# Optimization experiments

Hardware: AMD Instinct MI355X
Metric: run time of the kernel (lower is better)

The kernel has to match this reference:

```python
import jax, jax.numpy as jnp
import numpy as np

N = 50000      # num nodes
E = 1_600_000  # num edges
D = 64         # in_dim == hidden_dim
H = 4          # heads
C = 16         # head_dim = hidden_dim // heads
NEG = 0.2      # leaky_relu negative slope (PyG GATConv default)


def setup_inputs() -> dict:
    key = jax.random.key(0)
    ks = jax.random.split(key, 20)
    f = lambda k, s: (jax.random.normal(k, s, jnp.float32) * 0.1)
    return dict(
        node_features=jax.random.normal(ks[0], (N, D), jnp.float32),
        edge_index=jax.random.randint(ks[1], (2, E), 0, N, dtype=jnp.int32),
        edge_type=jax.random.randint(ks[2], (E,), 0, 5, dtype=jnp.int32),
        edge_attr=jax.random.normal(ks[3], (E, 1), jnp.float32),
        # GAT layer 1 (PyG GATConv: lin has no bias, att_* are [H,C], final bias [H*C])
        W1=f(ks[4], (D, H * C)), att_src1=f(ks[5], (H, C)), att_dst1=f(ks[6], (H, C)),
        We1=f(ks[7], (1, H * C)), att_e1=f(ks[8], (H, C)), b1=jnp.zeros((H * C,), jnp.float32),
        # GAT layer 2
        W2=f(ks[9], (D, H * C)), att_src2=f(ks[10], (H, C)), att_dst2=f(ks[11], (H, C)),
        We2=f(ks[12], (1, H * C)), att_e2=f(ks[13], (H, C)), b2=jnp.zeros((H * C,), jnp.float32),
        # LayerNorms
        g1=jnp.ones((D,), jnp.float32), beta1=jnp.zeros((D,), jnp.float32),
        g2=jnp.ones((D,), jnp.float32), beta2=jnp.zeros((D,), jnp.float32),
        # output head
        Wout=f(ks[14], (D, 1)), bout=jnp.zeros((1,), jnp.float32),
    )


def _layernorm(x, g, b, eps=1e-5):
    mu = x.mean(-1, keepdims=True)
    v = ((x - mu) ** 2).mean(-1, keepdims=True)
    return (x - mu) * jax.lax.rsqrt(v + eps) * g + b


def _seg_softmax(alpha, dst, n):
    # numerically stable segment softmax over incoming edges of each dst node
    m = jax.ops.segment_max(alpha, dst, num_segments=n)
    m = jnp.where(jnp.isfinite(m), m, 0.0)
    ex = jnp.exp(alpha - m[dst])
    den = jax.ops.segment_sum(ex, dst, num_segments=n)
    return ex / (den[dst] + 1e-16)


def _gatconv(x, src, dst, eattr, W, a_s, a_d, We, a_e, b, n):
    xs = (x @ W).reshape(n, H, C)                       # [N,H,C]
    a_src = jnp.einsum('nhc,hc->nh', xs, a_s)           # [N,H]
    a_dst = jnp.einsum('nhc,hc->nh', xs, a_d)           # [N,H]
    ee = (eattr @ We).reshape(-1, H, C)                 # [E',H,C]
    a_edge = jnp.einsum('ehc,hc->eh', ee, a_e)          # [E',H]
    alpha = a_src[src] + a_dst[dst] + a_edge            # [E',H]
    alpha = jax.nn.leaky_relu(alpha, NEG)
    alpha = _seg_softmax(alpha, dst, n)                 # [E',H]
    msg = xs[src] * alpha[..., None]                    # [E',H,C] gather-weighted messages
    out = jax.ops.segment_sum(msg, dst, num_segments=n) # scatter-aggregate
    return out.reshape(n, H * C) + b


def reference(node_features, edge_index, edge_type, edge_attr,
              W1, att_src1, att_dst1, We1, att_e1, b1,
              W2, att_src2, att_dst2, We2, att_e2, b2,
              g1, beta1, g2, beta2, Wout, bout):
    src, dst = edge_index[0], edge_index[1]
    # PyG add_self_loops(fill_value='mean'): self-loop edge_attr = mean of edge_attr over incoming edges
    cnt = jax.ops.segment_sum(jnp.ones((E,), jnp.float32), dst, num_segments=N)
    loop_attr = jax.ops.segment_sum(edge_attr, dst, num_segments=N) / jnp.maximum(cnt, 1.0)[:, None]
    loops = jnp.arange(N, dtype=src.dtype)
    src2 = jnp.concatenate([src, loops])
    dst2 = jnp.concatenate([dst, loops])
    ea = jnp.concatenate([edge_attr, loop_attr], axis=0)

    residual = node_features  # in_dim == hidden_dim -> no res_proj
    h = _gatconv(node_features, src2, dst2, ea, W1, att_src1, att_dst1, We1, att_e1, b1, N)
    h = jax.nn.elu(_layernorm(h + residual, g1, beta1))
    residual = h
    h = _gatconv(h, src2, dst2, ea, W2, att_src2, att_dst2, We2, att_e2, b2, N)
    h = jax.nn.elu(_layernorm(h + residual, g2, beta2))
    return h @ Wout + bout
```

## Files before the change

kernel.cpp:

```cpp
#include <hip/hip_runtime.h>
#include <hip/hip_bf16.h>
#include <cfloat>

#define NN 50000
#define NE 1600000
#define NEG 0.2f
#define NBKT 196
#define BNODE 256
#define P1_TILE 2048
#define P1_BLOCKS 782
#define GEMM_BLOCKS 782
#define BCAP 8704
#define SLOTS 96
#define L2E 1.4426950408889634f
#define SMEM_BYTES 10880

typedef __attribute__((ext_vector_type(8))) short bf8_t;
typedef __attribute__((ext_vector_type(4))) float f4_t;

__device__ __forceinline__ float bf16bits_to_f(unsigned v) {
  return __uint_as_float(v << 16);
}
__device__ __forceinline__ unsigned f_to_bf16bits(float f) {
  unsigned u = __float_as_uint(f);
  return (u + 0x7fffu + ((u >> 16) & 1u)) >> 16;
}

__device__ __forceinline__ bf8_t pack8(const float* p) {
  bf8_t r;
#pragma unroll
  for (int i = 0; i < 8; ++i) r[i] = (short)f_to_bf16bits(p[i]);
  return r;
}

__device__ void bin_body(char* smem, int blk, const int* __restrict__ src,
                         const int* __restrict__ dst,
                         const float* __restrict__ ea, int* __restrict__ gcnt,
                         int2* __restrict__ gbuf) {
  int* lcnt = (int*)smem;
  int* lcur = lcnt + NBKT;
  int t = threadIdx.x;
  if (t < NBKT) lcnt[t] = 0;
  __syncthreads();
  int e0 = blk * P1_TILE;
  int bb[8], vx[8], vy[8];
#pragma unroll
  for (int k = 0; k < 8; ++k) {
    int e = e0 + k * 256 + t;
    if (e < NE) {
      int d = dst[e];
      bb[k] = d >> 8;
      vx[k] = ((d & 255) << 16) | src[e];
      vy[k] = __float_as_int(ea[e]);
      atomicAdd(&lcnt[bb[k]], 1);
    } else {
      bb[k] = -1;
    }
  }
  __syncthreads();
  if (t < NBKT) lcur[t] = atomicAdd(&gcnt[t], lcnt[t]);
  __syncthreads();
#pragma unroll
  for (int k = 0; k < 8; ++k) {
    if (bb[k] >= 0) {
      int pos = atomicAdd(&lcur[bb[k]], 1);
      if (pos < BCAP) gbuf[(size_t)bb[k] * BCAP + pos] = make_int2(vx[k], vy[k]);
    }
  }
}

template <bool FP32IN>
__device__ void gemm_body(char* smem, int blk, const void* __restrict__ xin,
                          const float* __restrict__ W,
                          const float* __restrict__ att_s,
                          const float* __restrict__ att_d,
                          unsigned short* __restrict__ xsb,
                          float* __restrict__ a_src,
                          float* __restrict__ a_dst) {
  unsigned short(*Wt)[68] = (unsigned short(*)[68])smem;
  int t = threadIdx.x;
  for (int i = t; i < 4096; i += 256) {
    int k = i >> 6, n = i & 63;
    Wt[n][k] = (unsigned short)f_to_bf16bits(W[i]);
  }
  __syncthreads();
  {
    int k = t & 63, h = t >> 6;
    float ps = 0.f, pd = 0.f;
#pragma unroll
    for (int c = 0; c < 16; ++c) {
      float w = bf16bits_to_f(Wt[h * 16 + c][k]);
      ps = fmaf(w, att_s[h * 16 + c], ps);
      pd = fmaf(w, att_d[h * 16 + c], pd);
    }
    Wt[64 + h][k] = (unsigned short)f_to_bf16bits(ps * L2E);
    Wt[68 + h][k] = (unsigned short)f_to_bf16bits(pd * L2E);
    Wt[72 + h][k] = 0;
    Wt[76 + h][k] = 0;
  }
  __syncthreads();
  int lane = t & 63, wave = t >> 6;
  int quad = lane >> 4, n16 = lane & 15;

  bf8_t bfrag[5][2];
#pragma unroll
  for (int nt = 0; nt < 5; ++nt)
#pragma unroll
    for (int kk = 0; kk < 2; ++kk)
      bfrag[nt][kk] = *(const bf8_t*)&Wt[nt * 16 + n16][kk * 32 + quad * 8];

  int r0 = blk * 64 + wave * 16;
  int rowA = r0 + n16; if (rowA > NN - 1) rowA = NN - 1;
  bf8_t af0, af1;
  if (FP32IN) {
    const float* xr = (const float*)xin + (size_t)rowA * 64 + quad * 8;
    af0 = pack8(xr);
    af1 = pack8(xr + 32);
  } else {
    const bf8_t* xrow =
        (const bf8_t*)((const unsigned short*)xin + (size_t)rowA * 64);
    af0 = xrow[quad];
    af1 = xrow[4 + quad];
  }
#pragma unroll
  for (int nt = 0; nt < 5; ++nt) {
    f4_t acc = {0.f, 0.f, 0.f, 0.f};
    acc = __builtin_amdgcn_mfma_f32_16x16x32_bf16(af0, bfrag[nt][0], acc, 0, 0, 0);
    acc = __builtin_amdgcn_mfma_f32_16x16x32_bf16(af1, bfrag[nt][1], acc, 0, 0, 0);
    if (nt < 4) {
#pragma unroll
      for (int reg = 0; reg < 4; ++reg) {
        int row = r0 + quad * 4 + reg;
        if (row < NN)
          xsb[(size_t)row * 64 + nt * 16 + n16] =
              (unsigned short)f_to_bf16bits(acc[reg]);
      }
    } else {
#pragma unroll
      for (int reg = 0; reg < 4; ++reg) {
        int row = r0 + quad * 4 + reg;
        if (row < NN && n16 < 8) {
          if (n16 < 4) a_src[row * 4 + n16] = acc[reg];
          else a_dst[row * 4 + (n16 - 4)] = acc[reg];
        }
      }
    }
  }
}

__global__ __launch_bounds__(256) void front_kernel(
    const int* __restrict__ src, const int* __restrict__ dst,
    const float* __restrict__ ea, int* __restrict__ gcnt,
    int2* __restrict__ gbuf, const float* __restrict__ x,
    const float* __restrict__ W1, const float* __restrict__ as1,
    const float* __restrict__ ad1, unsigned short* __restrict__ xsb,
    float* __restrict__ a_src, float* __restrict__ a_dst) {
  __shared__ __align__(16) char smem[SMEM_BYTES];
  if (blockIdx.x < P1_BLOCKS) {
    bin_body(smem, blockIdx.x, src, dst, ea, gcnt, gbuf);
  } else {
    gemm_body<true>(smem, blockIdx.x - P1_BLOCKS, x, W1, as1, ad1, xsb, a_src,
                    a_dst);
  }
}

__global__ __launch_bounds__(256) void gemm2_kernel(
    const unsigned short* __restrict__ xin, const float* __restrict__ W,
    const float* __restrict__ att_s, const float* __restrict__ att_d,
    unsigned short* __restrict__ xsb, float* __restrict__ a_src,
    float* __restrict__ a_dst) {
  __shared__ __align__(16) char smem[SMEM_BYTES];
  gemm_body<false>(smem, blockIdx.x, xin, W, att_s, att_d, xsb, a_src, a_dst);
}

__global__ __launch_bounds__(1024) void build_kernel(
    const int* __restrict__ gcnt, const int2* __restrict__ gbuf,
    int* __restrict__ cnt, unsigned* __restrict__ csr) {
  __shared__ int lc[BNODE];
  int t = threadIdx.x;
  int b = blockIdx.x;
  if (t < BNODE) lc[t] = 0;
  __syncthreads();
  int len = gcnt[b]; if (len > BCAP) len = BCAP;
  const int2* buf = gbuf + (size_t)b * BCAP;
  for (int i = t; i < len; i += 1024) {
    int2 v = buf[i];
    int dl = (v.x >> 16) & 255;
    int s = v.x & 0xffff;
    int pos = atomicAdd(&lc[dl], 1);
    if (pos < SLOTS) {
      unsigned eb = ((unsigned)v.y) & 0xffff0000u;
      csr[(size_t)(b * BNODE + dl) * SLOTS + pos] = eb | (unsigned)s;
    }
  }
  __syncthreads();
  if (t < BNODE) {
    int n = b * BNODE + t;
    if (n < NN) cnt[n] = min(lc[t], SLOTS);
  }
}

template <bool HEAD>
__global__ __launch_bounds__(256) void aggregate_kernel(
    const int* __restrict__ cnt, const unsigned* __restrict__ csr,
    const unsigned short* __restrict__ xsb, const float* __restrict__ a_src,
    const float* __restrict__ a_dst, const float* __restrict__ We,
    const float* __restrict__ att_e, const float* __restrict__ bias,
    const void* __restrict__ resv, const float* __restrict__ g,
    const float* __restrict__ beta, const float* __restrict__ Wout,
    const float* __restrict__ bout, float* __restrict__ out,
    unsigned short* __restrict__ out_b) {
  __shared__ __align__(16) uint2 rec[4][64][4];
  int t = threadIdx.x;
  int lane = t & 63, wave = t >> 6;
  int n = blockIdx.x * 4 + wave;
  int d2 = lane & 31;
  int hb = d2 >> 3;
  int half = lane >> 5;

  float sp = We[lane] * att_e[lane];
#pragma unroll
  for (int off = 8; off; off >>= 1) sp += __shfl_xor(sp, off, 16);
  sp *= L2E;
  float s0 = __shfl(sp, 0, 64), s1 = __shfl(sp, 16, 64);
  float s2 = __shfl(sp, 32, 64), s3 = __shfl(sp, 48, 64);

  const float4 adv = *(const float4*)(a_dst + (size_t)n * 4);

  int dn = cnt[n];
  int r0 = n * SLOTS, r1 = r0 + dn;
  float accx = 0.f, accy = 0.f, den = 0.f, easum = 0.f;
  const uint2* rpb = &rec[wave][half][hb];
  const char* xd = (const char*)xsb + d2 * 4;

  for (int base = r0; base < r1; base += 64) {
    int c = r1 - base; if (c > 64) c = 64;
    int e = base + lane;
    unsigned ce = (e < r1) ? csr[e] : 0u;
    float ea = __uint_as_float(ce & 0xffff0000u);
    easum += ea;
    unsigned soff = (ce & 0xffffu) * 128u;
    float ex0 = 0.f, ex1 = 0.f, ex2 = 0.f, ex3 = 0.f;
    if (e < r1) {
      const float4 av = *(const float4*)(a_src + (size_t)(ce & 0xffffu) * 4);
      float a0 = av.x + fmaf(ea, s0, adv.x); a0 = fmaxf(a0, NEG * a0);
      float a1 = av.y + fmaf(ea, s1, adv.y); a1 = fmaxf(a1, NEG * a1);
      float a2 = av.z + fmaf(ea, s2, adv.z); a2 = fmaxf(a2, NEG * a2);
      float a3 = av.w + fmaf(ea, s3, adv.w); a3 = fmaxf(a3, NEG * a3);
      ex0 = exp2f(a0); ex1 = exp2f(a1); ex2 = exp2f(a2); ex3 = exp2f(a3);
    }
    uint4* wp = (uint4*)&rec[wave][lane][0];
    wp[0] = make_uint4(soff, __float_as_uint(ex0), soff, __float_as_uint(ex1));
    wp[1] = make_uint4(soff, __float_as_uint(ex2), soff, __float_as_uint(ex3));
    int c8 = (c + 7) & ~7;
    for (int j = 0; j < c8; j += 8) {
      uint2 va = rpb[j * 4];
      uint2 vb = rpb[j * 4 + 8];
      uint2 vc = rpb[j * 4 + 16];
      uint2 vd = rpb[j * 4 + 24];
      unsigned ua = *(const unsigned*)(xd + va.x);
      unsigned ub = *(const unsigned*)(xd + vb.x);
      unsigned uc = *(const unsigned*)(xd + vc.x);
      unsigned ud = *(const unsigned*)(xd + vd.x);
      float efa = __uint_as_float(va.y), efb = __uint_as_float(vb.y);
      float efc = __uint_as_float(vc.y), efd = __uint_as_float(vd.y);
      den += (efa + efb) + (efc + efd);
      accx = fmaf(efa, __uint_as_float(ua << 16), accx);
      accy = fmaf(efa, __uint_as_float(ua & 0xffff0000u), accy);
      accx = fmaf(efb, __uint_as_float(ub << 16), accx);
      accy = fmaf(efb, __uint_as_float(ub & 0xffff0000u), accy);
      accx = fmaf(efc, __uint_as_float(uc << 16), accx);
      accy = fmaf(efc, __uint_as_float(uc & 0xffff0000u), accy);
      accx = fmaf(efd, __uint_as_float(ud << 16), accx);
      accy = fmaf(efd, __uint_as_float(ud & 0xffff0000u), accy);
    }
  }

  den += __shfl_xor(den, 32, 64);
  accx += __shfl_xor(accx, 32, 64);
  accy += __shfl_xor(accy, 32, 64);
#pragma unroll
  for (int off = 32; off; off >>= 1) easum += __shfl_xor(easum, off, 64);

  float loop_ea = easum / fmaxf((float)dn, 1.0f);
  float as_h = a_src[(size_t)n * 4 + hb];
  float adn = (hb == 0) ? adv.x : (hb == 1) ? adv.y : (hb == 2) ? adv.z : adv.w;
  float sph = (hb == 0) ? s0 : (hb == 1) ? s1 : (hb == 2) ? s2 : s3;
  float a_self = as_h + fmaf(loop_ea, sph, adn);
  a_self = fmaxf(a_self, NEG * a_self);
  float ex_self = exp2f(a_self);
  den += ex_self;
  unsigned un = *(const unsigned*)((const char*)xsb + (size_t)n * 128 + d2 * 4);
  accx = fmaf(ex_self, __uint_as_float(un << 16), accx);
  accy = fmaf(ex_self, __uint_as_float(un & 0xffff0000u), accy);

  float rden = 1.f / (den + 1e-16f);
  const float2 bi = *(const float2*)(bias + d2 * 2);
  float2 rsd;
  if (HEAD) {
    unsigned ur =
        *(const unsigned*)((const unsigned short*)resv + (size_t)n * 64 + d2 * 2);
    rsd.x = bf16bits_to_f(ur & 0xffffu);
    rsd.y = __uint_as_float(ur & 0xffff0000u);
  } else {
    rsd = *(const float2*)((const float*)resv + (size_t)n * 64 + d2 * 2);
  }
  float vx = accx * rden + bi.x + rsd.x;
  float vy = accy * rden + bi.y + rsd.y;
  float s = vx + vy;
#pragma unroll
  for (int off = 32; off; off >>= 1) s += __shfl_xor(s, off, 64);
  float mu = s * (1.0f / 128.0f);
  float dx = vx - mu, dy = vy - mu;
  float var = dx * dx + dy * dy;
#pragma unroll
  for (int off = 32; off; off >>= 1) var += __shfl_xor(var, off, 64);
  var *= (1.0f / 128.0f);
  float rstd = rsqrtf(var + 1e-5f);
  const float2 gg = *(const float2*)(g + d2 * 2);
  const float2 bb = *(const float2*)(beta + d2 * 2);
  float yx = dx * rstd * gg.x + bb.x;
  float yy = dy * rstd * gg.y + bb.y;
  yx = yx > 0.f ? yx : expm1f(yx);
  yy = yy > 0.f ? yy : expm1f(yy);
  if (HEAD) {
    const float2 wv = *(const float2*)(Wout + d2 * 2);
    float p = yx * wv.x + yy * wv.y;
#pragma unroll
    for (int off = 32; off; off >>= 1) p += __shfl_xor(p, off, 64);
    if (lane == 0) out[n] = p * 0.5f + bout[0];
  } else if (lane < 32) {
    unsigned ob = f_to_bf16bits(yx) | (f_to_bf16bits(yy) << 16);
    *(unsigned*)(out_b + (size_t)n * 64 + d2 * 2) = ob;
  }
}

extern "C" void kernel_launch(void* const* d_in, const int* in_sizes, int n_in,
                              void* d_out, int out_size, void* d_ws,
                              size_t ws_size, hipStream_t stream) {
  const float* node_features = (const float*)d_in[0];
  const int* edge_index = (const int*)d_in[1];
  const int* src = edge_index;
  const int* dst = edge_index + NE;
  const float* edge_attr = (const float*)d_in[3];
  const float* W1 = (const float*)d_in[4];
  const float* att_src1 = (const float*)d_in[5];
  const float* att_dst1 = (const float*)d_in[6];
  const float* We1 = (const float*)d_in[7];
  const float* att_e1 = (const float*)d_in[8];
  const float* b1 = (const float*)d_in[9];
  const float* W2 = (const float*)d_in[10];
  const float* att_src2 = (const float*)d_in[11];
  const float* att_dst2 = (const float*)d_in[12];
  const float* We2 = (const float*)d_in[13];
  const float* att_e2 = (const float*)d_in[14];
  const float* b2 = (const float*)d_in[15];
  const float* g1 = (const float*)d_in[16];
  const float* beta1 = (const float*)d_in[17];
  const float* g2 = (const float*)d_in[18];
  const float* beta2 = (const float*)d_in[19];
  const float* Wout = (const float*)d_in[20];
  const float* bout = (const float*)d_in[21];
  float* out = (float*)d_out;

  char* ws = (char*)d_ws;
  size_t o = 0;
  auto alloc = [&](size_t bytes) {
    void* p = ws + o;
    o += (bytes + 255) & ~(size_t)255;
    return p;
  };
  int* gcnt = (int*)alloc((size_t)NBKT * 4);
  int2* gbuf = (int2*)alloc((size_t)NBKT * BCAP * 8);
  int* cnt = (int*)alloc((size_t)NN * 4);
  unsigned* csr = (unsigned*)alloc((size_t)NN * SLOTS * 4);
  unsigned short* xsb = (unsigned short*)alloc((size_t)NN * 64 * 2);
  unsigned short* h1b = (unsigned short*)alloc((size_t)NN * 64 * 2);
  float* a_srcb = (float*)alloc((size_t)NN * 4 * 4);
  float* a_dstb = (float*)alloc((size_t)NN * 4 * 4);

  hipMemsetAsync(gcnt, 0, (size_t)NBKT * 4, stream);

  front_kernel<<<P1_BLOCKS + GEMM_BLOCKS, 256, 0, stream>>>(
      src, dst, edge_attr, gcnt, gbuf, node_features, W1, att_src1, att_dst1,
      xsb, a_srcb, a_dstb);
  build_kernel<<<NBKT, 1024, 0, stream>>>(gcnt, gbuf, cnt, csr);

  aggregate_kernel<false><<<NN / 4, 256, 0, stream>>>(
      cnt, csr, xsb, a_srcb, a_dstb, We1, att_e1, b1, node_features, g1, beta1,
      nullptr, nullptr, nullptr, h1b);

  gemm2_kernel<<<GEMM_BLOCKS, 256, 0, stream>>>(h1b, W2, att_src2, att_dst2,
                                                xsb, a_srcb, a_dstb);
  aggregate_kernel<true><<<NN / 4, 256, 0, stream>>>(
      cnt, csr, xsb, a_srcb, a_dstb, We2, att_e2, b2, h1b, g2, beta2, Wout,
      bout, out, nullptr);
}
```

Measured before the change: 246.7 us.

## Process two nodes per wavefront in aggregation, one per half-wave

The aggregation kernel now assigns each 32-lane half of a wavefront to its own destination node, so a 256-thread block covers eight nodes and the grid is halved. Previously a whole wave served one node, with the two halves splitting that node's edge list and merging partial sums at the end. Edge loading, the gather loop, and the LayerNorm and output reductions are rewritten for 32-lane segments, which removes the cross-half merge and aims to raise lane utilisation when nodes have few incoming edges. The trade-off is divergence when the two nodes in a wave have different degrees, since both halves loop up to the larger count.

```diff
diff --git a/kernel.cpp b/kernel.cpp
--- a/kernel.cpp
+++ b/kernel.cpp
@@ -213,10 +213,10 @@
   __shared__ __align__(16) uint2 rec[4][64][4];
   int t = threadIdx.x;
   int lane = t & 63, wave = t >> 6;
-  int n = blockIdx.x * 4 + wave;
+  int half = lane >> 5;
   int d2 = lane & 31;
   int hb = d2 >> 3;
-  int half = lane >> 5;
+  int n = blockIdx.x * 8 + wave * 2 + half;
 
   float sp = We[lane] * att_e[lane];
 #pragma unroll
@@ -228,20 +228,20 @@
   const float4 adv = *(const float4*)(a_dst + (size_t)n * 4);
 
   int dn = cnt[n];
-  int r0 = n * SLOTS, r1 = r0 + dn;
+  int mdn = max(dn, __shfl_xor(dn, 32, 64));
   float accx = 0.f, accy = 0.f, den = 0.f, easum = 0.f;
-  const uint2* rpb = &rec[wave][half][hb];
+  const uint2* rpb = &rec[wave][half * 32][hb];
   const char* xd = (const char*)xsb + d2 * 4;
 
-  for (int base = r0; base < r1; base += 64) {
-    int c = r1 - base; if (c > 64) c = 64;
-    int e = base + lane;
-    unsigned ce = (e < r1) ? csr[e] : 0u;
+  for (int base = 0; base < mdn; base += 32) {
+    int c = mdn - base; if (c > 32) c = 32;
+    int el = base + d2;
+    unsigned ce = (el < dn) ? csr[(size_t)n * SLOTS + el] : 0u;
     float ea = __uint_as_float(ce & 0xffff0000u);
     easum += ea;
     unsigned soff = (ce & 0xffffu) * 128u;
     float ex0 = 0.f, ex1 = 0.f, ex2 = 0.f, ex3 = 0.f;
-    if (e < r1) {
+    if (el < dn) {
       const float4 av = *(const float4*)(a_src + (size_t)(ce & 0xffffu) * 4);
       float a0 = av.x + fmaf(ea, s0, adv.x); a0 = fmaxf(a0, NEG * a0);
       float a1 = av.y + fmaf(ea, s1, adv.y); a1 = fmaxf(a1, NEG * a1);
@@ -252,12 +252,12 @@
     uint4* wp = (uint4*)&rec[wave][lane][0];
     wp[0] = make_uint4(soff, __float_as_uint(ex0), soff, __float_as_uint(ex1));
     wp[1] = make_uint4(soff, __float_as_uint(ex2), soff, __float_as_uint(ex3));
-    int c8 = (c + 7) & ~7;
-    for (int j = 0; j < c8; j += 8) {
-      uint2 va = rpb[j * 4];
-      uint2 vb = rpb[j * 4 + 8];
-      uint2 vc = rpb[j * 4 + 16];
-      uint2 vd = rpb[j * 4 + 24];
+    int c8 = (c + 3) & ~3;
+    for (int j = 0; j < c8; j += 4) {
+      uint2 va = rpb[(j + 0) * 4];
+      uint2 vb = rpb[(j + 1) * 4];
+      uint2 vc = rpb[(j + 2) * 4];
+      uint2 vd = rpb[(j + 3) * 4];
       unsigned ua = *(const unsigned*)(xd + va.x);
       unsigned ub = *(const unsigned*)(xd + vb.x);
       unsigned uc = *(const unsigned*)(xd + vc.x);
@@ -276,11 +276,8 @@
     }
   }
 
-  den += __shfl_xor(den, 32, 64);
-  accx += __shfl_xor(accx, 32, 64);
-  accy += __shfl_xor(accy, 32, 64);
-#pragma unroll
-  for (int off = 32; off; off >>= 1) easum += __shfl_xor(easum, off, 64);
+#pragma unroll
+  for (int off = 16; off; off >>= 1) easum += __shfl_xor(easum, off, 32);
 
   float loop_ea = easum / fmaxf((float)dn, 1.0f);
   float as_h = a_src[(size_t)n * 4 + hb];
@@ -309,13 +306,13 @@
   float vy = accy * rden + bi.y + rsd.y;
   float s = vx + vy;
 #pragma unroll
-  for (int off = 32; off; off >>= 1) s += __shfl_xor(s, off, 64);
-  float mu = s * (1.0f / 128.0f);
+  for (int off = 16; off; off >>= 1) s += __shfl_xor(s, off, 32);
+  float mu = s * (1.0f / 64.0f);
   float dx = vx - mu, dy = vy - mu;
   float var = dx * dx + dy * dy;
 #pragma unroll
-  for (int off = 32; off; off >>= 1) var += __shfl_xor(var, off, 64);
-  var *= (1.0f / 128.0f);
+  for (int off = 16; off; off >>= 1) var += __shfl_xor(var, off, 32);
+  var *= (1.0f / 64.0f);
   float rstd = rsqrtf(var + 1e-5f);
   const float2 gg = *(const float2*)(g + d2 * 2);
   const float2 bb = *(const float2*)(beta + d2 * 2);
@@ -327,9 +324,9 @@
     const float2 wv = *(const float2*)(Wout + d2 * 2);
     float p = yx * wv.x + yy * wv.y;
 #pragma unroll
-    for (int off = 32; off; off >>= 1) p += __shfl_xor(p, off, 64);
-    if (lane == 0) out[n] = p * 0.5f + bout[0];
-  } else if (lane < 32) {
+    for (int off = 16; off; off >>= 1) p += __shfl_xor(p, off, 32);
+    if (d2 == 0) out[n] = p + bout[0];
+  } else {
     unsigned ob = f_to_bf16bits(yx) | (f_to_bf16bits(yy) << 16);
     *(unsigned*)(out_b + (size_t)n * 64 + d2 * 2) = ob;
   }
@@ -386,13 +383,13 @@
       xsb, a_srcb, a_dstb);
   build_kernel<<<NBKT, 1024, 0, stream>>>(gcnt, gbuf, cnt, csr);
 
-  aggregate_kernel<false><<<NN / 4, 256, 0, stream>>>(
+  aggregate_kernel<false><<<NN / 8, 256, 0, stream>>>(
       cnt, csr, xsb, a_srcb, a_dstb, We1, att_e1, b1, node_features, g1, beta1,
       nullptr, nullptr, nullptr, h1b);
 
   gemm2_kernel<<<GEMM_BLOCKS, 256, 0, stream>>>(h1b, W2, att_src2, att_dst2,
                                                 xsb, a_srcb, a_dstb);
-  aggregate_kernel<true><<<NN / 4, 256, 0, stream>>>(
+  aggregate_kernel<true><<<NN / 8, 256, 0, stream>>>(
       cnt, csr, xsb, a_srcb, a_dstb, We2, att_e2, b2, h1b, g2, beta2, Wout,
       bout, out, nullptr);
 }
```

Result: faster. 239.2 us (-3.1%).
